# Optimization experiments

Measured on AMD Instinct MI355X. Metric: run time of the kernel, lower is better.

The kernel has to match this reference:

```python
import jax, jax.numpy as jnp
import numpy as np

N_NODES = 100000
N_EDGES = 1600000
IN_DIM, HID_DIM, OUT_DIM = 512, 128, 64
BN_EPS = 1e-5


def setup_inputs() -> dict:
    key = jax.random.key(0)
    ks = jax.random.split(key, 8)
    x = jax.random.normal(ks[0], (N_NODES, IN_DIM), dtype=jnp.float32)
    edge_index = jax.random.randint(ks[1], (2, N_EDGES), 0, N_NODES, dtype=jnp.int64)
    W1 = jax.random.normal(ks[2], (IN_DIM, HID_DIM), dtype=jnp.float32) / np.sqrt(IN_DIM)
    b1 = jnp.zeros((HID_DIM,), dtype=jnp.float32)
    W2 = jax.random.normal(ks[3], (HID_DIM, OUT_DIM), dtype=jnp.float32) / np.sqrt(HID_DIM)
    b2 = jnp.zeros((OUT_DIM,), dtype=jnp.float32)
    gamma = jnp.ones((HID_DIM,), dtype=jnp.float32)
    beta = jnp.zeros((HID_DIM,), dtype=jnp.float32)
    return {"x": x, "edge_index": edge_index, "W1": W1, "b1": b1,
            "W2": W2, "b2": b2, "gamma": gamma, "beta": beta}


def _gcn_conv(x, src, dst, W, b):
    # PyG GCNConv(normalize=False): transform then sum-aggregate src->dst, no self-loops
    h = x @ W                                   # [N, out]
    agg = jax.ops.segment_sum(h[src], dst, num_segments=N_NODES)
    return agg + b


def _batchnorm(h, gamma, beta):
    mean = jnp.mean(h, axis=0)
    var = jnp.mean(jnp.square(h - mean), axis=0)  # biased var (training mode)
    return (h - mean) * jax.lax.rsqrt(var + BN_EPS) * gamma + beta


def reference(x, edge_index, W1, b1, W2, b2, gamma, beta):
    src, dst = edge_index[0], edge_index[1]
    h = _gcn_conv(x, src, dst, W1, b1)          # [N, HID]
    h = _batchnorm(h, gamma, beta)
    h = jax.nn.relu(h)
    h = _gcn_conv(h, src, dst, W2, b2)          # [N, OUT]
    # F.normalize(p=2, dim=1), eps=1e-12
    norm = jnp.linalg.norm(h, axis=1, keepdims=True)
    return h / jnp.maximum(norm, 1e-12)
```

## Files before the change

### kernel.cpp

```cpp
#include <hip/hip_runtime.h>
#include <hip/hip_bf16.h>
#include <stdint.h>

#define NN 100000
#define NE 1600000
#define IND 512
#define HID 128
#define OUTD 64
#define BN_EPS 1e-5f
#define NP 98
#define PSZ 1024
#define PCAP 20480
#define BINCH 8192
#define NBIN 196

typedef __attribute__((ext_vector_type(8))) short short8v;
typedef __attribute__((ext_vector_type(4))) float f32x4;

__device__ __forceinline__ ushort f2bf(float f, float& back) {
  uint u = __float_as_uint(f);
  uint r = u + 0x7FFFu + ((u >> 16) & 1u);
  ushort h = (ushort)(r >> 16);
  back = __uint_as_float(((uint)h) << 16);
  return h;
}
__device__ __forceinline__ ushort f2bf_n(float f) {
  uint u = __float_as_uint(f);
  uint r = u + 0x7FFFu + ((u >> 16) & 1u);
  return (ushort)(r >> 16);
}
__device__ __forceinline__ float bf2f(ushort h) {
  return __uint_as_float(((uint)h) << 16);
}
__device__ __forceinline__ uint packbf(float lo, float hi) {
  return (uint)f2bf_n(lo) | ((uint)f2bf_n(hi) << 16);
}

__device__ __forceinline__ int edge_at(const int* e32, int f, int i) {
  if (f) return (int)((const long long*)e32)[i];
  return e32[i];
}

__global__ __launch_bounds__(256) void k_prep(const int* __restrict__ edges,
                                              const float* __restrict__ W1,
                                              const float* __restrict__ W2,
                                              int* __restrict__ flag,
                                              ushort* __restrict__ Wth,
                                              ushort* __restrict__ Wtl,
                                              ushort* __restrict__ W2th,
                                              ushort* __restrict__ W2tl) {
  const int bid = blockIdx.x, tid = threadIdx.x;
  if (bid == 0) {
    __shared__ int nz;
    if (tid == 0) nz = 0;
    __syncthreads();
    if (tid < 64) {
      int v = edges[2 * tid + 1];
      if (v != 0) atomicAdd(&nz, 1);
    }
    __syncthreads();
    if (tid == 0) *flag = (nz == 0) ? 1 : 0;
    return;
  }
  if (bid <= 256) {
    int i = (bid - 1) * 256 + tid;
    int n = i >> 9, k = i & 511;
    float w = W1[(size_t)k * HID + n];
    float back;
    Wth[i] = f2bf(w, back);
    Wtl[i] = f2bf_n(w - back);
    return;
  }
  {
    int j = (bid - 257) * 256 + tid;
    int n = j >> 7, k = j & 127;
    float w = W2[(size_t)k * OUTD + n];
    float back;
    W2th[j] = f2bf(w, back);
    W2tl[j] = f2bf_n(w - back);
  }
}

__device__ void bin_body(int bid, ushort* smem16, const int* edges,
                         const int* flag, int* gCursor, int* staging) {
  int* cnt   = (int*)smem16;
  int* scn   = cnt + 128;
  int* base  = cnt + 256;
  int* cur   = cnt + 384;
  int* items = cnt + 512;
  const int tid = threadIdx.x;
  const int e0 = bid * BINCH;
  const int ecnt = min(BINCH, NE - e0);
  const int f = *flag;
  for (int i = tid; i < NP; i += 256) cnt[i] = 0;
  __syncthreads();
  for (int i = tid; i < ecnt; i += 256) {
    int d = edge_at(edges, f, NE + e0 + i);
    atomicAdd(&cnt[d >> 10], 1);
  }
  __syncthreads();
  if (tid == 0) {
    int s = 0;
    for (int p = 0; p < NP; ++p) { scn[p] = s; s += cnt[p]; }
  }
  __syncthreads();
  if (tid < NP) {
    base[tid] = (cnt[tid] > 0) ? atomicAdd(&gCursor[tid], cnt[tid]) : 0;
    cur[tid] = 0;
  }
  __syncthreads();
  for (int i = tid; i < ecnt; i += 256) {
    int d = edge_at(edges, f, NE + e0 + i);
    int s = edge_at(edges, f, e0 + i);
    int p = d >> 10;
    int lp = atomicAdd(&cur[p], 1);
    items[scn[p] + lp] = (s << 10) | (d & (PSZ - 1));
  }
  __syncthreads();
  for (int p = 0; p < NP; ++p) {
    int c = cnt[p];
    if (c == 0) continue;
    int gb = base[p];
    int* dst = staging + (size_t)p * PCAP;
    for (int i = tid; i < c; i += 256) {
      int gpos = gb + i;
      if (gpos < PCAP) dst[gpos] = items[scn[p] + i];
    }
  }
}

__device__ void gemm1_body(int bid, ushort* smem, const float* x,
                           const ushort* Wth, const ushort* Wtl,
                           ushort* h1b) {
  ushort* sOut = smem;
  const int tid = threadIdx.x;
  const int lane = tid & 63, wid = tid >> 6;
  const int wr = wid >> 1, wc = wid & 1;
  const int lrow = lane & 15, lkg = lane >> 4;
  const int row0 = bid * 128;

  f32x4 acc[4][4];
#pragma unroll
  for (int m = 0; m < 4; ++m)
#pragma unroll
    for (int n = 0; n < 4; ++n) acc[m][n] = (f32x4){0.f, 0.f, 0.f, 0.f};

  float4 ra[4];
  uint4 rbh[2], rbl[2];

#pragma unroll
  for (int i = 0; i < 4; ++i) {
    int flat = i * 256 + tid, r = flat >> 3, kq = flat & 7;
    int grow = row0 + r; if (grow > NN - 1) grow = NN - 1;
    ra[i] = *(const float4*)(x + (size_t)grow * IND + kq * 4);
  }
#pragma unroll
  for (int i = 0; i < 2; ++i) {
    int flat = i * 256 + tid, col = flat >> 2, kc = flat & 3;
    rbh[i] = *(const uint4*)(Wth + (size_t)col * IND + kc * 8);
    rbl[i] = *(const uint4*)(Wtl + (size_t)col * IND + kc * 8);
  }
  {
    ushort* dAh = smem;
    ushort* dBh = smem + 5120;
    ushort* dBl = smem + 10240;
#pragma unroll
    for (int i = 0; i < 4; ++i) {
      int flat = i * 256 + tid, r = flat >> 3, kq = flat & 7;
      ushort4 hi;
      hi.x = f2bf_n(ra[i].x); hi.y = f2bf_n(ra[i].y);
      hi.z = f2bf_n(ra[i].z); hi.w = f2bf_n(ra[i].w);
      *(ushort4*)&dAh[r * 40 + kq * 4] = hi;
    }
#pragma unroll
    for (int i = 0; i < 2; ++i) {
      int flat = i * 256 + tid, col = flat >> 2, kc = flat & 3;
      *(uint4*)&dBh[col * 40 + kc * 8] = rbh[i];
      *(uint4*)&dBl[col * 40 + kc * 8] = rbl[i];
    }
  }

  int cur = 0;
  for (int s = 0; s < 16; ++s) {
    __syncthreads();
    if (s < 15) {
      int kt = (s + 1) * 32;
#pragma unroll
      for (int i = 0; i < 4; ++i) {
        int flat = i * 256 + tid, r = flat >> 3, kq = flat & 7;
        int grow = row0 + r; if (grow > NN - 1) grow = NN - 1;
        ra[i] = *(const float4*)(x + (size_t)grow * IND + kt + kq * 4);
      }
#pragma unroll
      for (int i = 0; i < 2; ++i) {
        int flat = i * 256 + tid, col = flat >> 2, kc = flat & 3;
        rbh[i] = *(const uint4*)(Wth + (size_t)col * IND + kt + kc * 8);
        rbl[i] = *(const uint4*)(Wtl + (size_t)col * IND + kt + kc * 8);
      }
    }
    {
      const ushort* bAh = smem + cur * 15360;
      const ushort* bBh = bAh + 5120;
      const ushort* bBl = bAh + 10240;
      short8v ah[4], bh[4], bl[4];
#pragma unroll
      for (int m = 0; m < 4; ++m) {
        int r = wr * 64 + m * 16 + lrow;
        ah[m] = *(const short8v*)&bAh[r * 40 + lkg * 8];
      }
#pragma unroll
      for (int n = 0; n < 4; ++n) {
        int c = wc * 64 + n * 16 + lrow;
        bh[n] = *(const short8v*)&bBh[c * 40 + lkg * 8];
        bl[n] = *(const short8v*)&bBl[c * 40 + lkg * 8];
      }
#pragma unroll
      for (int m = 0; m < 4; ++m)
#pragma unroll
        for (int n = 0; n < 4; ++n) {
          acc[m][n] = __builtin_amdgcn_mfma_f32_16x16x32_bf16(ah[m], bh[n], acc[m][n], 0, 0, 0);
          acc[m][n] = __builtin_amdgcn_mfma_f32_16x16x32_bf16(ah[m], bl[n], acc[m][n], 0, 0, 0);
        }
    }
    if (s < 15) {
      ushort* dAh = smem + (cur ^ 1) * 15360;
      ushort* dBh = dAh + 5120;
      ushort* dBl = dAh + 10240;
#pragma unroll
      for (int i = 0; i < 4; ++i) {
        int flat = i * 256 + tid, r = flat >> 3, kq = flat & 7;
        ushort4 hi;
        hi.x = f2bf_n(ra[i].x); hi.y = f2bf_n(ra[i].y);
        hi.z = f2bf_n(ra[i].z); hi.w = f2bf_n(ra[i].w);
        *(ushort4*)&dAh[r * 40 + kq * 4] = hi;
      }
#pragma unroll
      for (int i = 0; i < 2; ++i) {
        int flat = i * 256 + tid, col = flat >> 2, kc = flat & 3;
        *(uint4*)&dBh[col * 40 + kc * 8] = rbh[i];
        *(uint4*)&dBl[col * 40 + kc * 8] = rbl[i];
      }
    }
    cur ^= 1;
  }

  __syncthreads();
#pragma unroll
  for (int m = 0; m < 4; ++m)
#pragma unroll
    for (int i = 0; i < 4; ++i) {
      int lr = wr * 64 + m * 16 + lkg * 4 + i;
#pragma unroll
      for (int n = 0; n < 4; ++n)
        sOut[lr * 136 + wc * 64 + n * 16 + lrow] = f2bf_n(acc[m][n][i]);
    }
  __syncthreads();
#pragma unroll
  for (int j = 0; j < 8; ++j) {
    int flat = j * 256 + tid;
    int r = flat >> 4, c = flat & 15;
    int grow = row0 + r;
    if (grow < NN)
      *(uint4*)(h1b + (size_t)grow * HID + c * 8) =
          *(const uint4*)&sOut[r * 136 + c * 8];
  }
}

__global__ __launch_bounds__(256) void k_fused1(const float* __restrict__ x,
                                                const ushort* __restrict__ Wth,
                                                const ushort* __restrict__ Wtl,
                                                const int* __restrict__ edges,
                                                const int* __restrict__ flag,
                                                int* __restrict__ gCursor,
                                                int* __restrict__ staging,
                                                ushort* __restrict__ h1b) {
  __shared__ __align__(16) ushort smem[30720];
  if (blockIdx.x < NBIN)
    bin_body(blockIdx.x, smem, edges, flag, gCursor, staging);
  else
    gemm1_body(blockIdx.x - NBIN, smem, x, Wth, Wtl, h1b);
}

__global__ void k_partscan(const int* __restrict__ gCursor,
                           int* __restrict__ partBase, int* __restrict__ offsets) {
  __shared__ int s[128];
  int tid = threadIdx.x;
  int v = (tid < NP) ? min(gCursor[tid], PCAP) : 0;
  s[tid] = v;
  __syncthreads();
  for (int off = 1; off < 128; off <<= 1) {
    int t = (tid >= off) ? s[tid - off] : 0;
    __syncthreads();
    s[tid] += t;
    __syncthreads();
  }
  if (tid < NP) partBase[tid] = s[tid] - v;
  if (tid == 0) { partBase[NP] = NE; offsets[NN] = NE; }
}

__global__ __launch_bounds__(256) void k_csrpart(const int* __restrict__ staging,
                                                 const int* __restrict__ gCursor,
                                                 const int* __restrict__ partBase,
                                                 int* __restrict__ offsets,
                                                 int* __restrict__ csr_src) {
  __shared__ int cnt[PSZ];
  __shared__ int cur[PSZ];
  __shared__ int tsum[256];
  __shared__ int srcbuf[PCAP];
  const int tid = threadIdx.x;
  const int p = blockIdx.x;
  const int tot = min(gCursor[p], PCAP);
  const int gbase = partBase[p];
  const int* st = staging + (size_t)p * PCAP;
  for (int i = tid; i < PSZ; i += 256) { cnt[i] = 0; cur[i] = 0; }
  __syncthreads();
  for (int i = tid; i < tot; i += 256) atomicAdd(&cnt[st[i] & (PSZ - 1)], 1);
  __syncthreads();
  int b0 = tid * 4;
  int c0 = cnt[b0], c1 = cnt[b0 + 1], c2 = cnt[b0 + 2], c3 = cnt[b0 + 3];
  int ls = c0 + c1 + c2 + c3;
  tsum[tid] = ls;
  __syncthreads();
  for (int off = 1; off < 256; off <<= 1) {
    int t = (tid >= off) ? tsum[tid - off] : 0;
    __syncthreads();
    tsum[tid] += t;
    __syncthreads();
  }
  int ebase = tsum[tid] - ls;
  cnt[b0] = ebase;
  cnt[b0 + 1] = ebase + c0;
  cnt[b0 + 2] = ebase + c0 + c1;
  cnt[b0 + 3] = ebase + c0 + c1 + c2;
  __syncthreads();
  for (int i = tid; i < PSZ; i += 256) {
    int node = p * PSZ + i;
    if (node < NN) offsets[node] = gbase + cnt[i];
  }
  for (int i = tid; i < tot; i += 256) {
    int item = st[i];
    int dl = item & (PSZ - 1);
    int lp = atomicAdd(&cur[dl], 1);
    srcbuf[cnt[dl] + lp] = item >> 10;
  }
  __syncthreads();
  for (int i = tid; i < tot; i += 256) csr_src[gbase + i] = srcbuf[i];
}

__global__ __launch_bounds__(256) void k_agg1(const ushort* __restrict__ h1b,
                                              const int* __restrict__ offsets,
                                              const int* __restrict__ csr_src,
                                              const float* __restrict__ b1,
                                              ushort* __restrict__ aggb) {
  int w = threadIdx.x >> 6, lane = threadIdx.x & 63;
  int n = blockIdx.x * 4 + w;
  if (n >= NN) return;
  int beg = offsets[n], end = offsets[n + 1];
  const uint* h = (const uint*)h1b;
  float2 a0 = ((const float2*)b1)[lane];
  float2 a1 = {0.f, 0.f};
  int i = beg;
  for (; i + 3 < end; i += 4) {
    uint v0 = h[(size_t)csr_src[i] * 64 + lane];
    uint v1 = h[(size_t)csr_src[i + 1] * 64 + lane];
    uint v2 = h[(size_t)csr_src[i + 2] * 64 + lane];
    uint v3 = h[(size_t)csr_src[i + 3] * 64 + lane];
    a0.x += __uint_as_float(v0 << 16) + __uint_as_float(v1 << 16);
    a0.y += __uint_as_float(v0 & 0xffff0000u) + __uint_as_float(v1 & 0xffff0000u);
    a1.x += __uint_as_float(v2 << 16) + __uint_as_float(v3 << 16);
    a1.y += __uint_as_float(v2 & 0xffff0000u) + __uint_as_float(v3 & 0xffff0000u);
  }
  for (; i < end; ++i) {
    uint v = h[(size_t)csr_src[i] * 64 + lane];
    a0.x += __uint_as_float(v << 16);
    a0.y += __uint_as_float(v & 0xffff0000u);
  }
  a0.x += a1.x; a0.y += a1.y;
  ((uint*)aggb)[(size_t)n * 64 + lane] = packbf(a0.x, a0.y);
}

__global__ __launch_bounds__(256) void k_bnstats(const ushort* __restrict__ aggb,
                                                 float* __restrict__ gsum,
                                                 float* __restrict__ gsq) {
  __shared__ float2 ss[4][64], qq[4][64];
  int tid = threadIdx.x;
  int lane = tid & 63, g = tid >> 6;
  int r0 = blockIdx.x * 128;
  const uint* a = (const uint*)aggb;
  float2 s = {0.f, 0.f}, q = {0.f, 0.f};
  for (int k = 0; k < 32; ++k) {
    int r = r0 + g + 4 * k;
    if (r < NN) {
      uint v = a[(size_t)r * 64 + lane];
      float lo = __uint_as_float(v << 16);
      float hi = __uint_as_float(v & 0xffff0000u);
      s.x += lo; s.y += hi;
      q.x += lo * lo; q.y += hi * hi;
    }
  }
  ss[g][lane] = s; qq[g][lane] = q;
  __syncthreads();
  if (g == 0) {
    float2 S = ss[0][lane], Q = qq[0][lane];
#pragma unroll
    for (int gg = 1; gg < 4; ++gg) {
      S.x += ss[gg][lane].x; S.y += ss[gg][lane].y;
      Q.x += qq[gg][lane].x; Q.y += qq[gg][lane].y;
    }
    atomicAdd(&gsum[2 * lane], S.x);
    atomicAdd(&gsum[2 * lane + 1], S.y);
    atomicAdd(&gsq[2 * lane], Q.x);
    atomicAdd(&gsq[2 * lane + 1], Q.y);
  }
}

__global__ void k_bnfin(const float* __restrict__ gsum, const float* __restrict__ gsq,
                        const float* __restrict__ gamma, const float* __restrict__ beta,
                        float* __restrict__ isg, float* __restrict__ bb) {
  int c = threadIdx.x;
  float mean = gsum[c] * (1.f / NN);
  float var = gsq[c] * (1.f / NN) - mean * mean;
  var = fmaxf(var, 0.f);
  float inv = 1.f / sqrtf(var + BN_EPS);
  float g = gamma[c] * inv;
  isg[c] = g;
  bb[c] = beta[c] - mean * g;
}

__global__ __launch_bounds__(256) void k_gemm2m(const ushort* __restrict__ aggb,
                                                const ushort* __restrict__ W2th,
                                                const ushort* __restrict__ W2tl,
                                                const float* __restrict__ isg,
                                                const float* __restrict__ bb,
                                                ushort* __restrict__ h2b) {
  __shared__ __align__(16) ushort smem[27648];
  __shared__ float isgS[128], bbS[128];
  ushort* sBh = smem;
  ushort* sBl = smem + 8704;
  ushort* sA  = smem + 17408;
  ushort* sOut = sA;
  const int tid = threadIdx.x;
  const int lane = tid & 63, wid = tid >> 6;
  const int wr = wid >> 1, wc = wid & 1;
  const int lrow = lane & 15, lkg = lane >> 4;
  const int row0 = blockIdx.x * 128;

  if (tid < 128) { isgS[tid] = isg[tid]; bbS[tid] = bb[tid]; }
#pragma unroll
  for (int i = 0; i < 4; ++i) {
    int c = i * 256 + tid;
    int n = c >> 4, kq = c & 15;
    *(uint4*)&sBh[n * 136 + kq * 8] = *(const uint4*)(W2th + (size_t)n * HID + kq * 8);
    *(uint4*)&sBl[n * 136 + kq * 8] = *(const uint4*)(W2tl + (size_t)n * HID + kq * 8);
  }

  f32x4 acc[4][2];
#pragma unroll
  for (int m = 0; m < 4; ++m)
#pragma unroll
    for (int n = 0; n < 2; ++n) acc[m][n] = (f32x4){0.f, 0.f, 0.f, 0.f};

  uint4 rA[2];
#pragma unroll
  for (int i = 0; i < 2; ++i) {
    int c = i * 256 + tid;
    int r = c >> 2, cq = c & 3;
    int grow = row0 + r; if (grow > NN - 1) grow = NN - 1;
    rA[i] = *(const uint4*)(aggb + (size_t)grow * HID + cq * 8);
  }
  __syncthreads();

  {
    ushort* dA = sA;
#pragma unroll
    for (int i = 0; i < 2; ++i) {
      int c = i * 256 + tid;
      int r = c >> 2, cq = c & 3;
      int k0 = cq * 8;
      uint4 v = rA[i];
      uint o[4];
      const uint* vv = (const uint*)&v;
#pragma unroll
      for (int j = 0; j < 4; ++j) {
        float lo = __uint_as_float(vv[j] << 16);
        float hi = __uint_as_float(vv[j] & 0xffff0000u);
        lo = fmaxf(fmaf(lo, isgS[k0 + 2 * j], bbS[k0 + 2 * j]), 0.f);
        hi = fmaxf(fmaf(hi, isgS[k0 + 2 * j + 1], bbS[k0 + 2 * j + 1]), 0.f);
        o[j] = packbf(lo, hi);
      }
      *(uint4*)&dA[r * 40 + cq * 8] = *(const uint4*)o;
    }
  }

  int cur = 0;
  for (int s = 0; s < 4; ++s) {
    __syncthreads();
    const int kt = s * 32;
    if (s < 3) {
      int ktn = kt + 32;
#pragma unroll
      for (int i = 0; i < 2; ++i) {
        int c = i * 256 + tid;
        int r = c >> 2, cq = c & 3;
        int grow = row0 + r; if (grow > NN - 1) grow = NN - 1;
        rA[i] = *(const uint4*)(aggb + (size_t)grow * HID + ktn + cq * 8);
      }
    }
    {
      const ushort* bA = sA + cur * 5120;
      short8v ah[4], bh[2], bl[2];
#pragma unroll
      for (int m = 0; m < 4; ++m) {
        int r = wr * 64 + m * 16 + lrow;
        ah[m] = *(const short8v*)&bA[r * 40 + lkg * 8];
      }
#pragma unroll
      for (int n = 0; n < 2; ++n) {
        int c = wc * 32 + n * 16 + lrow;
        bh[n] = *(const short8v*)&sBh[c * 136 + kt + lkg * 8];
        bl[n] = *(const short8v*)&sBl[c * 136 + kt + lkg * 8];
      }
#pragma unroll
      for (int m = 0; m < 4; ++m)
#pragma unroll
        for (int n = 0; n < 2; ++n) {
          acc[m][n] = __builtin_amdgcn_mfma_f32_16x16x32_bf16(ah[m], bh[n], acc[m][n], 0, 0, 0);
          acc[m][n] = __builtin_amdgcn_mfma_f32_16x16x32_bf16(ah[m], bl[n], acc[m][n], 0, 0, 0);
        }
    }
    if (s < 3) {
      ushort* dA = sA + (cur ^ 1) * 5120;
      int k0b = (s + 1) * 32;
#pragma unroll
      for (int i = 0; i < 2; ++i) {
        int c = i * 256 + tid;
        int r = c >> 2, cq = c & 3;
        int k0 = k0b + cq * 8;
        uint4 v = rA[i];
        uint o[4];
        const uint* vv = (const uint*)&v;
#pragma unroll
        for (int j = 0; j < 4; ++j) {
          float lo = __uint_as_float(vv[j] << 16);
          float hi = __uint_as_float(vv[j] & 0xffff0000u);
          lo = fmaxf(fmaf(lo, isgS[k0 + 2 * j], bbS[k0 + 2 * j]), 0.f);
          hi = fmaxf(fmaf(hi, isgS[k0 + 2 * j + 1], bbS[k0 + 2 * j + 1]), 0.f);
          o[j] = packbf(lo, hi);
        }
        *(uint4*)&dA[r * 40 + cq * 8] = *(const uint4*)o;
      }
    }
    cur ^= 1;
  }

  __syncthreads();
#pragma unroll
  for (int m = 0; m < 4; ++m)
#pragma unroll
    for (int i = 0; i < 4; ++i) {
      int lr = wr * 64 + m * 16 + lkg * 4 + i;
#pragma unroll
      for (int n = 0; n < 2; ++n)
        sOut[lr * 72 + wc * 32 + n * 16 + lrow] = f2bf_n(acc[m][n][i]);
    }
  __syncthreads();
#pragma unroll
  for (int i = 0; i < 4; ++i) {
    int c = i * 256 + tid;
    int r = c >> 3, cq = c & 7;
    int grow = row0 + r;
    if (grow < NN)
      *(uint4*)(h2b + (size_t)grow * OUTD + cq * 8) =
          *(const uint4*)&sOut[r * 72 + cq * 8];
  }
}

__global__ __launch_bounds__(256) void k_agg2norm(const ushort* __restrict__ h2b,
                                                  const int* __restrict__ offsets,
                                                  const int* __restrict__ csr_src,
                                                  const float* __restrict__ b2,
                                                  float* __restrict__ out) {
  int w = threadIdx.x >> 6, lane = threadIdx.x & 63;
  int n = blockIdx.x * 4 + w;
  if (n >= NN) return;
  int beg = offsets[n], end = offsets[n + 1];
  float a0 = b2[lane], a1 = 0.f;
  int i = beg;
  for (; i + 3 < end; i += 4) {
    a0 += bf2f(h2b[(size_t)csr_src[i] * OUTD + lane]) +
          bf2f(h2b[(size_t)csr_src[i + 1] * OUTD + lane]);
    a1 += bf2f(h2b[(size_t)csr_src[i + 2] * OUTD + lane]) +
          bf2f(h2b[(size_t)csr_src[i + 3] * OUTD + lane]);
  }
  for (; i < end; ++i) a0 += bf2f(h2b[(size_t)csr_src[i] * OUTD + lane]);
  float acc = a0 + a1;
  float q = acc * acc;
#pragma unroll
  for (int off = 32; off > 0; off >>= 1) q += __shfl_xor(q, off);
  float norm = sqrtf(q);
  float scale = 1.f / fmaxf(norm, 1e-12f);
  out[(size_t)n * OUTD + lane] = acc * scale;
}

extern "C" void kernel_launch(void* const* d_in, const int* in_sizes, int n_in,
                              void* d_out, int out_size, void* d_ws, size_t ws_size,
                              hipStream_t stream) {
  const float* x     = (const float*)d_in[0];
  const int*   edges = (const int*)d_in[1];
  const float* W1    = (const float*)d_in[2];
  const float* b1    = (const float*)d_in[3];
  const float* W2    = (const float*)d_in[4];
  const float* b2    = (const float*)d_in[5];
  const float* gamma = (const float*)d_in[6];
  const float* beta  = (const float*)d_in[7];

  char* ws = (char*)d_ws;
  ushort* h1b     = (ushort*)(ws);
  ushort* aggb    = (ushort*)(ws + 26000000);
  int*    csr_src = (int*)(ws + 77500000);
  int*    offsets = (int*)(ws + 84000000);
  int*    staging = (int*)(ws + 84400128);
  int*    gCursor = (int*)(ws + 92428544);
  int*    partBase= (int*)(ws + 92429056);
  float*  gsum    = (float*)(ws + 92429568);
  float*  gsq     = (float*)(ws + 92430080);
  float*  isg     = (float*)(ws + 92430592);
  float*  bbv     = (float*)(ws + 92431104);
  int*    eflag   = (int*)(ws + 92431616);
  ushort* Wth     = (ushort*)(ws + 92432128);
  ushort* Wtl     = (ushort*)(ws + 92563200);
  ushort* W2th    = (ushort*)(ws + 92694272);
  ushort* W2tl    = (ushort*)(ws + 92710656);
  ushort* h2b     = h1b;

  if (ws_size < 92727040) return;

  hipMemsetAsync(gCursor, 0, 2048, stream);

  k_prep<<<289, 256, 0, stream>>>(edges, W1, W2, eflag, Wth, Wtl, W2th, W2tl);
  k_fused1<<<NBIN + 782, 256, 0, stream>>>(x, Wth, Wtl, edges, eflag,
                                           gCursor, staging, h1b);
  k_partscan<<<1, 128, 0, stream>>>(gCursor, partBase, offsets);
  k_csrpart<<<NP, 256, 0, stream>>>(staging, gCursor, partBase, offsets, csr_src);
  k_agg1<<<25000, 256, 0, stream>>>(h1b, offsets, csr_src, b1, aggb);
  k_bnstats<<<782, 256, 0, stream>>>(aggb, gsum, gsq);
  k_bnfin<<<1, 128, 0, stream>>>(gsum, gsq, gamma, beta, isg, bbv);
  k_gemm2m<<<782, 256, 0, stream>>>(aggb, W2th, W2tl, isg, bbv, h2b);
  k_agg2norm<<<25000, 256, 0, stream>>>(h2b, offsets, csr_src, b2,
                                        (float*)d_out);
}
```

Measured before the change: 315.3 us.

## Fold scan and BN-finalize kernels into consumers; split warp across edges in aggregations

Removes the single-block partition-scan kernel by having each CSR-partition block sum preceding partition counts itself. It also removes the BN finalize kernel by computing scale and shift inside each GEMM2 block. In both aggregation kernels, each 64-lane wavefront now handles two edges at once: each half-wave reads a whole row with wider per-lane loads, then the halves are combined with a cross-half shuffle. This cuts launch count and doubles memory-level parallelism per gather, at the cost of redundant small scans and BN math in every block, plus idle lanes on the final store.

```diff
diff --git a/kernel.cpp b/kernel.cpp
--- a/kernel.cpp
+++ b/kernel.cpp
@@ -32,6 +32,8 @@
 __device__ __forceinline__ float bf2f(ushort h) {
   return __uint_as_float(((uint)h) << 16);
 }
+__device__ __forceinline__ float bflo(uint v) { return __uint_as_float(v << 16); }
+__device__ __forceinline__ float bfhi(uint v) { return __uint_as_float(v & 0xffff0000u); }
 __device__ __forceinline__ uint packbf(float lo, float hi) {
   return (uint)f2bf_n(lo) | ((uint)f2bf_n(hi) << 16);
 }
@@ -281,39 +283,28 @@
     gemm1_body(blockIdx.x - NBIN, smem, x, Wth, Wtl, h1b);
 }
 
-__global__ void k_partscan(const int* __restrict__ gCursor,
-                           int* __restrict__ partBase, int* __restrict__ offsets) {
-  __shared__ int s[128];
-  int tid = threadIdx.x;
-  int v = (tid < NP) ? min(gCursor[tid], PCAP) : 0;
-  s[tid] = v;
-  __syncthreads();
-  for (int off = 1; off < 128; off <<= 1) {
-    int t = (tid >= off) ? s[tid - off] : 0;
-    __syncthreads();
-    s[tid] += t;
-    __syncthreads();
-  }
-  if (tid < NP) partBase[tid] = s[tid] - v;
-  if (tid == 0) { partBase[NP] = NE; offsets[NN] = NE; }
-}
-
 __global__ __launch_bounds__(256) void k_csrpart(const int* __restrict__ staging,
                                                  const int* __restrict__ gCursor,
-                                                 const int* __restrict__ partBase,
                                                  int* __restrict__ offsets,
                                                  int* __restrict__ csr_src) {
   __shared__ int cnt[PSZ];
   __shared__ int cur[PSZ];
   __shared__ int tsum[256];
   __shared__ int srcbuf[PCAP];
+  __shared__ int gbase_s;
   const int tid = threadIdx.x;
   const int p = blockIdx.x;
+  if (tid == 0) {
+    int s = 0;
+    for (int q = 0; q < p; ++q) s += min(gCursor[q], PCAP);
+    gbase_s = s;
+    if (p == NP - 1) offsets[NN] = NE;
+  }
   const int tot = min(gCursor[p], PCAP);
-  const int gbase = partBase[p];
   const int* st = staging + (size_t)p * PCAP;
   for (int i = tid; i < PSZ; i += 256) { cnt[i] = 0; cur[i] = 0; }
   __syncthreads();
+  const int gbase = gbase_s;
   for (int i = tid; i < tot; i += 256) atomicAdd(&cnt[st[i] & (PSZ - 1)], 1);
   __syncthreads();
   int b0 = tid * 4;
@@ -356,27 +347,32 @@
   int n = blockIdx.x * 4 + w;
   if (n >= NN) return;
   int beg = offsets[n], end = offsets[n + 1];
-  const uint* h = (const uint*)h1b;
-  float2 a0 = ((const float2*)b1)[lane];
-  float2 a1 = {0.f, 0.f};
-  int i = beg;
-  for (; i + 3 < end; i += 4) {
-    uint v0 = h[(size_t)csr_src[i] * 64 + lane];
-    uint v1 = h[(size_t)csr_src[i + 1] * 64 + lane];
-    uint v2 = h[(size_t)csr_src[i + 2] * 64 + lane];
-    uint v3 = h[(size_t)csr_src[i + 3] * 64 + lane];
-    a0.x += __uint_as_float(v0 << 16) + __uint_as_float(v1 << 16);
-    a0.y += __uint_as_float(v0 & 0xffff0000u) + __uint_as_float(v1 & 0xffff0000u);
-    a1.x += __uint_as_float(v2 << 16) + __uint_as_float(v3 << 16);
-    a1.y += __uint_as_float(v2 & 0xffff0000u) + __uint_as_float(v3 & 0xffff0000u);
-  }
-  for (; i < end; ++i) {
-    uint v = h[(size_t)csr_src[i] * 64 + lane];
-    a0.x += __uint_as_float(v << 16);
-    a0.y += __uint_as_float(v & 0xffff0000u);
-  }
-  a0.x += a1.x; a0.y += a1.y;
-  ((uint*)aggb)[(size_t)n * 64 + lane] = packbf(a0.x, a0.y);
+  int half = lane >> 5, ch = lane & 31;
+  const uint2* h = (const uint2*)h1b;
+  float4 a = {0.f, 0.f, 0.f, 0.f}, a2 = {0.f, 0.f, 0.f, 0.f};
+  int i = beg + half;
+  for (; i + 2 < end; i += 4) {
+    uint2 v0 = h[(size_t)csr_src[i] * 32 + ch];
+    uint2 v1 = h[(size_t)csr_src[i + 2] * 32 + ch];
+    a.x += bflo(v0.x); a.y += bfhi(v0.x); a.z += bflo(v0.y); a.w += bfhi(v0.y);
+    a2.x += bflo(v1.x); a2.y += bfhi(v1.x); a2.z += bflo(v1.y); a2.w += bfhi(v1.y);
+  }
+  if (i < end) {
+    uint2 v = h[(size_t)csr_src[i] * 32 + ch];
+    a.x += bflo(v.x); a.y += bfhi(v.x); a.z += bflo(v.y); a.w += bfhi(v.y);
+  }
+  a.x += a2.x; a.y += a2.y; a.z += a2.z; a.w += a2.w;
+  a.x += __shfl_xor(a.x, 32);
+  a.y += __shfl_xor(a.y, 32);
+  a.z += __shfl_xor(a.z, 32);
+  a.w += __shfl_xor(a.w, 32);
+  if (half == 0) {
+    float4 b = *(const float4*)(b1 + 4 * ch);
+    uint2 o;
+    o.x = packbf(a.x + b.x, a.y + b.y);
+    o.y = packbf(a.z + b.z, a.w + b.w);
+    ((uint2*)aggb)[(size_t)n * 32 + ch] = o;
+  }
 }
 
 __global__ __launch_bounds__(256) void k_bnstats(const ushort* __restrict__ aggb,
@@ -392,8 +388,7 @@
     int r = r0 + g + 4 * k;
     if (r < NN) {
       uint v = a[(size_t)r * 64 + lane];
-      float lo = __uint_as_float(v << 16);
-      float hi = __uint_as_float(v & 0xffff0000u);
+      float lo = bflo(v), hi = bfhi(v);
       s.x += lo; s.y += hi;
       q.x += lo * lo; q.y += hi * hi;
     }
@@ -414,24 +409,13 @@
   }
 }
 
-__global__ void k_bnfin(const float* __restrict__ gsum, const float* __restrict__ gsq,
-                        const float* __restrict__ gamma, const float* __restrict__ beta,
-                        float* __restrict__ isg, float* __restrict__ bb) {
-  int c = threadIdx.x;
-  float mean = gsum[c] * (1.f / NN);
-  float var = gsq[c] * (1.f / NN) - mean * mean;
-  var = fmaxf(var, 0.f);
-  float inv = 1.f / sqrtf(var + BN_EPS);
-  float g = gamma[c] * inv;
-  isg[c] = g;
-  bb[c] = beta[c] - mean * g;
-}
-
 __global__ __launch_bounds__(256) void k_gemm2m(const ushort* __restrict__ aggb,
                                                 const ushort* __restrict__ W2th,
                                                 const ushort* __restrict__ W2tl,
-                                                const float* __restrict__ isg,
-                                                const float* __restrict__ bb,
+                                                const float* __restrict__ gsum,
+                                                const float* __restrict__ gsq,
+                                                const float* __restrict__ gamma,
+                                                const float* __restrict__ beta,
                                                 ushort* __restrict__ h2b) {
   __shared__ __align__(16) ushort smem[27648];
   __shared__ float isgS[128], bbS[128];
@@ -445,7 +429,14 @@
   const int lrow = lane & 15, lkg = lane >> 4;
   const int row0 = blockIdx.x * 128;
 
-  if (tid < 128) { isgS[tid] = isg[tid]; bbS[tid] = bb[tid]; }
+  if (tid < 128) {
+    float mean = gsum[tid] * (1.f / NN);
+    float var = fmaxf(gsq[tid] * (1.f / NN) - mean * mean, 0.f);
+    float inv = 1.f / sqrtf(var + BN_EPS);
+    float g = gamma[tid] * inv;
+    isgS[tid] = g;
+    bbS[tid] = beta[tid] - mean * g;
+  }
 #pragma unroll
   for (int i = 0; i < 4; ++i) {
     int c = i * 256 + tid;
@@ -482,8 +473,7 @@
       const uint* vv = (const uint*)&v;
 #pragma unroll
       for (int j = 0; j < 4; ++j) {
-        float lo = __uint_as_float(vv[j] << 16);
-        float hi = __uint_as_float(vv[j] & 0xffff0000u);
+        float lo = bflo(vv[j]), hi = bfhi(vv[j]);
         lo = fmaxf(fmaf(lo, isgS[k0 + 2 * j], bbS[k0 + 2 * j]), 0.f);
         hi = fmaxf(fmaf(hi, isgS[k0 + 2 * j + 1], bbS[k0 + 2 * j + 1]), 0.f);
         o[j] = packbf(lo, hi);
@@ -541,8 +531,7 @@
         const uint* vv = (const uint*)&v;
 #pragma unroll
         for (int j = 0; j < 4; ++j) {
-          float lo = __uint_as_float(vv[j] << 16);
-          float hi = __uint_as_float(vv[j] & 0xffff0000u);
+          float lo = bflo(vv[j]), hi = bfhi(vv[j]);
           lo = fmaxf(fmaf(lo, isgS[k0 + 2 * j], bbS[k0 + 2 * j]), 0.f);
           hi = fmaxf(fmaf(hi, isgS[k0 + 2 * j + 1], bbS[k0 + 2 * j + 1]), 0.f);
           o[j] = packbf(lo, hi);
@@ -584,22 +573,34 @@
   int n = blockIdx.x * 4 + w;
   if (n >= NN) return;
   int beg = offsets[n], end = offsets[n + 1];
-  float a0 = b2[lane], a1 = 0.f;
-  int i = beg;
-  for (; i + 3 < end; i += 4) {
-    a0 += bf2f(h2b[(size_t)csr_src[i] * OUTD + lane]) +
-          bf2f(h2b[(size_t)csr_src[i + 1] * OUTD + lane]);
-    a1 += bf2f(h2b[(size_t)csr_src[i + 2] * OUTD + lane]) +
-          bf2f(h2b[(size_t)csr_src[i + 3] * OUTD + lane]);
-  }
-  for (; i < end; ++i) a0 += bf2f(h2b[(size_t)csr_src[i] * OUTD + lane]);
-  float acc = a0 + a1;
-  float q = acc * acc;
-#pragma unroll
-  for (int off = 32; off > 0; off >>= 1) q += __shfl_xor(q, off);
+  int half = lane >> 5, ch = lane & 31;
+  const uint* h = (const uint*)h2b;
+  float2 a = {0.f, 0.f}, a2 = {0.f, 0.f};
+  int i = beg + half;
+  for (; i + 2 < end; i += 4) {
+    uint v0 = h[(size_t)csr_src[i] * 32 + ch];
+    uint v1 = h[(size_t)csr_src[i + 2] * 32 + ch];
+    a.x += bflo(v0); a.y += bfhi(v0);
+    a2.x += bflo(v1); a2.y += bfhi(v1);
+  }
+  if (i < end) {
+    uint v = h[(size_t)csr_src[i] * 32 + ch];
+    a.x += bflo(v); a.y += bfhi(v);
+  }
+  a.x += a2.x; a.y += a2.y;
+  a.x += __shfl_xor(a.x, 32);
+  a.y += __shfl_xor(a.y, 32);
+  float2 b = *(const float2*)(b2 + 2 * ch);
+  a.x += b.x; a.y += b.y;
+  float q = a.x * a.x + a.y * a.y;
+#pragma unroll
+  for (int off = 16; off > 0; off >>= 1) q += __shfl_xor(q, off);
   float norm = sqrtf(q);
   float scale = 1.f / fmaxf(norm, 1e-12f);
-  out[(size_t)n * OUTD + lane] = acc * scale;
+  if (half == 0) {
+    float2 o = {a.x * scale, a.y * scale};
+    *(float2*)(out + (size_t)n * OUTD + 2 * ch) = o;
+  }
 }
 
 extern "C" void kernel_launch(void* const* d_in, const int* in_sizes, int n_in,
@@ -624,14 +625,13 @@
   int*    partBase= (int*)(ws + 92429056);
   float*  gsum    = (float*)(ws + 92429568);
   float*  gsq     = (float*)(ws + 92430080);
-  float*  isg     = (float*)(ws + 92430592);
-  float*  bbv     = (float*)(ws + 92431104);
   int*    eflag   = (int*)(ws + 92431616);
   ushort* Wth     = (ushort*)(ws + 92432128);
   ushort* Wtl     = (ushort*)(ws + 92563200);
   ushort* W2th    = (ushort*)(ws + 92694272);
   ushort* W2tl    = (ushort*)(ws + 92710656);
   ushort* h2b     = h1b;
+  (void)partBase;
 
   if (ws_size < 92727040) return;
 
@@ -640,12 +640,10 @@
   k_prep<<<289, 256, 0, stream>>>(edges, W1, W2, eflag, Wth, Wtl, W2th, W2tl);
   k_fused1<<<NBIN + 782, 256, 0, stream>>>(x, Wth, Wtl, edges, eflag,
                                            gCursor, staging, h1b);
-  k_partscan<<<1, 128, 0, stream>>>(gCursor, partBase, offsets);
-  k_csrpart<<<NP, 256, 0, stream>>>(staging, gCursor, partBase, offsets, csr_src);
+  k_csrpart<<<NP, 256, 0, stream>>>(staging, gCursor, offsets, csr_src);
   k_agg1<<<25000, 256, 0, stream>>>(h1b, offsets, csr_src, b1, aggb);
   k_bnstats<<<782, 256, 0, stream>>>(aggb, gsum, gsq);
-  k_bnfin<<<1, 128, 0, stream>>>(gsum, gsq, gamma, beta, isg, bbv);
-  k_gemm2m<<<782, 256, 0, stream>>>(aggb, W2th, W2tl, isg, bbv, h2b);
+  k_gemm2m<<<782, 256, 0, stream>>>(aggb, W2th, W2tl, gsum, gsq, gamma, beta, h2b);
   k_agg2norm<<<25000, 256, 0, stream>>>(h2b, offsets, csr_src, b2,
                                         (float*)d_out);
 }
```

Result: no change. 309.5 us (-1.8%).
